# Optimization experiments

Measured on AMD Instinct MI355X. Metric: run time of the kernel, lower is better.

Reference implementation:

```python
import jax, jax.numpy as jnp
import numpy as np

D_X, N_LAYERS, N_HEADS, D_OUT = 1024, 4, 16, 1024
D_H = D_X // N_HEADS
LN_EPS = 1e-5


def _layernorm(x, g, b):
    mu = jnp.mean(x, axis=-1, keepdims=True)
    var = jnp.var(x, axis=-1, keepdims=True)
    return (x - mu) * jax.lax.rsqrt(var + LN_EPS) * g + b


def setup_inputs() -> dict:
    key = jax.random.key(0)
    ks = jax.random.split(key, 12)
    s = 0.02
    inp = {
        "x": jax.random.normal(ks[0], (4, 1024, D_X), dtype=jnp.float32),
        # per-layer, per-head K/V projections (Q is unused by the original math)
        "Wk": jax.random.normal(ks[1], (N_LAYERS, N_HEADS, D_X, D_H), dtype=jnp.float32) * s,
        "bk": jnp.zeros((N_LAYERS, N_HEADS, D_H), dtype=jnp.float32),
        "Wv": jax.random.normal(ks[2], (N_LAYERS, N_HEADS, D_X, D_H), dtype=jnp.float32) * s,
        "bv": jnp.zeros((N_LAYERS, N_HEADS, D_H), dtype=jnp.float32),
        # per-layer FFN linear
        "Wl": jax.random.normal(ks[3], (N_LAYERS, D_X, D_X), dtype=jnp.float32) * s,
        "bl": jnp.zeros((N_LAYERS, D_X), dtype=jnp.float32),
        # per-layer LayerNorm params
        "g1": jnp.ones((N_LAYERS, D_X), dtype=jnp.float32),
        "b1": jnp.zeros((N_LAYERS, D_X), dtype=jnp.float32),
        "g2": jnp.ones((N_LAYERS, D_X), dtype=jnp.float32),
        "b2": jnp.zeros((N_LAYERS, D_X), dtype=jnp.float32),
        # output projection
        "Wo": jax.random.normal(ks[4], (D_X, D_OUT), dtype=jnp.float32) * s,
        "bo": jnp.zeros((D_OUT,), dtype=jnp.float32),
    }
    return inp


def reference(x, Wk, bk, Wv, bv, Wl, bl, g1, b1, g2, b2, Wo, bo):
    B, S, _ = x.shape
    scale = 1.0 / np.sqrt(D_H).astype(np.float32)
    for l in range(N_LAYERS):
        # batched across heads instead of the original per-head Python loop
        K = jnp.einsum("bsd,hdk->bhsk", x, Wk[l]) + bk[l][None, :, None, :]
        V = jnp.einsum("bsd,hdk->bhsk", x, Wv[l]) + bv[l][None, :, None, :]
        # faithful quirk: logits = K @ V^T (Q is never used in the source)
        logits = jnp.einsum("bhsk,bhtk->bhst", K, V) * scale
        attn = jnp.einsum("bhst,bhtk->bhsk", jax.nn.softmax(logits, axis=-1), V)
        attn = attn.transpose(0, 2, 1, 3).reshape(B, S, D_X)  # concat heads
        x = _layernorm(x + attn, g1[l], b1[l])
        ff = jax.nn.relu(jnp.einsum("bsd,de->bse", x, Wl[l]) + bl[l])
        x = _layernorm(x + ff, g2[l], b2[l])
    return jnp.einsum("bsd,do->bso", x, Wo) + bo
```

## Files before the change

### kernel.cpp

```cpp
#include <hip/hip_runtime.h>

typedef unsigned short u16;
typedef unsigned int u32;
typedef __attribute__((ext_vector_type(4))) float f32x4;
typedef __attribute__((ext_vector_type(8))) short short8;

#if __has_builtin(__builtin_amdgcn_exp2f)
#define EXP2(x) __builtin_amdgcn_exp2f(x)
#else
#define EXP2(x) exp2f(x)
#endif

#define SCALEK 0.18033688011112042f

__device__ __forceinline__ u16 f2b(float f) {
    unsigned u = __float_as_uint(f);
    u += 0x7fff + ((u >> 16) & 1);
    return (u16)(u >> 16);
}
__device__ __forceinline__ float b2f(u16 v) {
    return __uint_as_float(((unsigned)v) << 16);
}
__device__ __forceinline__ int swz(int byteoff) {
    return byteoff ^ (((byteoff >> 7) & 7) << 4);
}
__device__ __forceinline__ int swzV(int byteoff) {
    return byteoff ^ (((byteoff >> 8) & 7) << 4);
}
__device__ __forceinline__ void gl16(const u16* g, u16* l) {
    __builtin_amdgcn_global_load_lds(
        (const __attribute__((address_space(1))) unsigned*)(g),
        (__attribute__((address_space(3))) unsigned*)(l), 16, 0, 0);
}
__device__ __forceinline__ u32 cvtpk(float lo, float hi) {
    u32 r;
    asm("v_cvt_pk_bf16_f32 %0, %1, %2" : "=v"(r) : "v"(lo), "v"(hi));
    return r;
}
__device__ __forceinline__ void plswap(u32& a, u32& b) {
    asm("v_permlane32_swap_b32 %0, %1" : "+v"(a), "+v"(b));
    asm("v_permlane16_swap_b32 %0, %1" : "+v"(a), "+v"(b));
}
#define MFMA16(a, b, c) __builtin_amdgcn_mfma_f32_16x16x32_bf16((a), (b), (c), 0, 0, 0)

__global__ __launch_bounds__(256) void pack_wkv_t(const float* __restrict__ W,
                                                  u16* __restrict__ out, int voff) {
    __shared__ float tile[32][33];
    int z = blockIdx.z; int l = z >> 4, h = z & 15;
    const float* ip = W + (size_t)z * 1024 * 64;
    u16* op = out + (size_t)l * 2048 * 1024 + (size_t)(voff + h * 64) * 1024;
    int tx = threadIdx.x & 31, ty = threadIdx.x >> 5;
    int d0 = blockIdx.y * 32, k0 = blockIdx.x * 32;
#pragma unroll
    for (int j = 0; j < 32; j += 8)
        tile[ty + j][tx] = ip[(size_t)(d0 + ty + j) * 64 + k0 + tx];
    __syncthreads();
#pragma unroll
    for (int j = 0; j < 32; j += 8)
        op[(size_t)(k0 + ty + j) * 1024 + d0 + tx] = f2b(tile[tx][ty + j]);
}

__global__ __launch_bounds__(256) void transpose_cvt(const float* __restrict__ in,
                                                     u16* __restrict__ out, int R, int C) {
    __shared__ float tile[32][33];
    const float* ip = in + (size_t)blockIdx.z * R * C;
    u16* op = out + (size_t)blockIdx.z * R * C;
    int tx = threadIdx.x & 31, ty = threadIdx.x >> 5;
    int r0 = blockIdx.y * 32, c0 = blockIdx.x * 32;
#pragma unroll
    for (int j = 0; j < 32; j += 8)
        tile[ty + j][tx] = ip[(size_t)(r0 + ty + j) * C + c0 + tx];
    __syncthreads();
#pragma unroll
    for (int j = 0; j < 32; j += 8)
        op[(size_t)(c0 + ty + j) * R + r0 + tx] = f2b(tile[tx][ty + j]);
}

__global__ __launch_bounds__(256) void cvt_bf16(const float* __restrict__ in,
                                                u16* __restrict__ out, int n) {
    int i = (blockIdx.x * 256 + threadIdx.x) * 4;
    if (i >= n) return;
    float4 v = *(const float4*)&in[i];
    ushort4 o = {f2b(v.x), f2b(v.y), f2b(v.z), f2b(v.w)};
    *(ushort4*)&out[i] = o;
}

template <int EPI, int BN>
__global__ __launch_bounds__(256) void gemm_bt(const u16* __restrict__ A,
                                               const u16* __restrict__ B,
                                               const float* __restrict__ bias1,
                                               const float* __restrict__ bias2, int split,
                                               void* __restrict__ Cv,
                                               u16* __restrict__ VTout,
                                               int M, int N, int K) {
    constexpr int NB = BN / 32;
    constexpr int NLB = BN / 32;
    constexpr int L2BN = (BN == 128) ? 7 : 6;
    __shared__ __align__(16) u16 lA[2][128 * 64];
    __shared__ __align__(16) u16 lB[2][BN * 64];
    const int t = threadIdx.x;
    const int lane = t & 63, w = t >> 6;
    const int wr = w >> 1, wc = w & 1;
    const int g = lane >> 4, r = lane & 15;
    const int bid = blockIdx.x;
    const int rgn = bid & 7, idx = bid >> 3;
    const int by = (rgn >> 1) * 8 + (idx >> 3);
    const int bx = (rgn & 1) * 8 + (idx & 7);
    const int m0 = by * 128, n0 = bx * BN;

    const u16* sA[4];
    const u16* sB[NLB];
#pragma unroll
    for (int j = 0; j < 4; ++j) {
        int c = j * 256 + t;
        sA[j] = A + (size_t)(m0 + (c & 127)) * K + (c >> 7) * 8;
    }
#pragma unroll
    for (int j = 0; j < NLB; ++j) {
        int c = j * 256 + t;
        sB[j] = B + (size_t)(n0 + (c & (BN - 1))) * K + (c >> L2BN) * 8;
    }

    f32x4 zero4 = {0.f, 0.f, 0.f, 0.f};
    f32x4 acc[4][NB];
#pragma unroll
    for (int m = 0; m < 4; ++m)
#pragma unroll
        for (int n = 0; n < NB; ++n) acc[m][n] = zero4;

#define GSTAGE(bufi, k0)                                                 \
    do {                                                                 \
        _Pragma("unroll") for (int j = 0; j < 4; ++j)                    \
            gl16(sA[j] + (k0), &lA[bufi][(j * 256 + w * 64) * 8]);       \
        _Pragma("unroll") for (int j = 0; j < NLB; ++j)                  \
            gl16(sB[j] + (k0), &lB[bufi][(j * 256 + w * 64) * 8]);       \
    } while (0)

    GSTAGE(0, 0);
    __syncthreads();
    const int nk = K >> 6;
    for (int kt = 0; kt < nk; ++kt) {
        const int cur = kt & 1;
        if (kt + 1 < nk) GSTAGE(cur ^ 1, (kt + 1) * 64);
#pragma unroll
        for (int ks = 0; ks < 2; ++ks) {
            short8 af[4], bf[NB];
#pragma unroll
            for (int m = 0; m < 4; ++m)
                af[m] = *(const short8*)&lA[cur][((ks * 4 + g) * 128 + wr * 64 + m * 16 + r) * 8];
#pragma unroll
            for (int n = 0; n < NB; ++n)
                bf[n] = *(const short8*)&lB[cur][((ks * 4 + g) * BN + wc * (BN / 2) + n * 16 + r) * 8];
#pragma unroll
            for (int m = 0; m < 4; ++m)
#pragma unroll
                for (int n = 0; n < NB; ++n)
                    acc[m][n] = MFMA16(af[m], bf[n], acc[m][n]);
        }
        __syncthreads();
    }
#undef GSTAGE

#pragma unroll
    for (int m = 0; m < 4; ++m) {
        int row = m0 + wr * 64 + m * 16 + g * 4;
#pragma unroll
        for (int n = 0; n < NB; ++n) {
            int col = n0 + wc * (BN / 2) + n * 16 + r;
            float bv_ = (col < split) ? bias1[col] : bias2[col - split];
            if (EPI == 0) {
                float sc = (col < split) ? SCALEK : 1.0f;
                ushort4 qv;
                qv.x = f2b((acc[m][n][0] + bv_) * sc);
                qv.y = f2b((acc[m][n][1] + bv_) * sc);
                qv.z = f2b((acc[m][n][2] + bv_) * sc);
                qv.w = f2b((acc[m][n][3] + bv_) * sc);
                u16* Cb = (u16*)Cv;
                Cb[(size_t)(row + 0) * N + col] = qv.x;
                Cb[(size_t)(row + 1) * N + col] = qv.y;
                Cb[(size_t)(row + 2) * N + col] = qv.z;
                Cb[(size_t)(row + 3) * N + col] = qv.w;
                if (col >= split) {
                    int d = col - split, b_ = row >> 10, s = row & 1023;
                    *(ushort4*)&VTout[(((size_t)(b_ * 16) + (d >> 6)) * 64 + (d & 63)) * 1024 + s] = qv;
                }
            } else if (EPI == 1) {
                u16* Cb = (u16*)Cv;
#pragma unroll
                for (int i = 0; i < 4; ++i)
                    Cb[(size_t)(row + i) * N + col] = f2b(fmaxf(acc[m][n][i] + bv_, 0.f));
            } else {
#pragma unroll
                for (int i = 0; i < 4; ++i)
                    ((float*)Cv)[(size_t)(row + i) * N + col] = acc[m][n][i] + bv_;
            }
        }
    }
}

__global__ __launch_bounds__(512) void attn_kernel(const u16* __restrict__ KV,
                                                   const u16* __restrict__ VT,
                                                   u16* __restrict__ Out) {
    __shared__ __align__(16) u16 kt[2][1024 * 8];
    __shared__ __align__(16) u16 vt[2][1024 * 8];
    const int t = threadIdx.x;
    const int lane = t & 63, w = t >> 6;
    const int g = lane >> 4, r = lane & 15;
    const int d0 = blockIdx.x;
    const int q = d0 >> 3;
    const int bh = (d0 & 7) * 8 + (q >> 3), qb = q & 7;
    const int h = bh & 15, b = bh >> 4;
    const u16* Kbase = KV + (size_t)b * 1024 * 2048 + h * 64;
    const u16* Vbase = Kbase + 1024;
    const u16* VTbase = VT + ((size_t)(b * 16 + h)) * 64 * 1024;

    const int qrow = qb * 128 + w * 16 + r;
    const short8 qf0 = *(const short8*)&Kbase[(size_t)qrow * 2048 + g * 8];
    const short8 qf1 = *(const short8*)&Kbase[(size_t)qrow * 2048 + 32 + g * 8];

    const int krow1 = t >> 3;
    const int kcol = ((((t & 7) * 16) ^ ((krow1 & 7) << 4)) >> 1);
    const u16* Ks1 = Vbase + (size_t)krow1 * 2048 + kcol;
    const u16* Ks2 = Vbase + (size_t)(64 + krow1) * 2048 + kcol;
    const int vrow1 = t >> 4;
    const int vcol = ((((t & 15) * 16) ^ ((vrow1 & 7) << 4)) >> 1);
    const u16* Vs1 = VTbase + (size_t)vrow1 * 1024 + vcol;
    const u16* Vs2 = VTbase + (size_t)(32 + vrow1) * 1024 + vcol;

#define STAGE(bufi, t0)                                              \
    do {                                                             \
        gl16(Ks1 + (size_t)(t0) * 2048, &kt[bufi][(w * 64) * 8]);    \
        gl16(Ks2 + (size_t)(t0) * 2048, &kt[bufi][(512 + w * 64) * 8]); \
        gl16(Vs1 + (t0), &vt[bufi][(w * 64) * 8]);                   \
        gl16(Vs2 + (t0), &vt[bufi][(512 + w * 64) * 8]);             \
    } while (0)

    STAGE(0, 0);

    float m = -1e30f, l = 0.f;
    f32x4 zero4 = {0.f, 0.f, 0.f, 0.f};
    f32x4 oacc[4];
#pragma unroll
    for (int n = 0; n < 4; ++n) oacc[n] = zero4;
    const int cbase = (lane & 48) | (g << 2);
    __syncthreads();

    for (int tt = 0; tt < 8; ++tt) {
        const int cur = tt & 1;
        if (tt < 7) STAGE(cur ^ 1, (tt + 1) * 128);
        const char* kbuf = (const char*)&kt[cur][0];
        const char* vbuf = (const char*)&vt[cur][0];

        f32x4 sfT[8];
#pragma unroll
        for (int n = 0; n < 8; ++n) sfT[n] = zero4;
#pragma unroll
        for (int ks = 0; ks < 2; ++ks) {
            const short8 qf = ks ? qf1 : qf0;
#pragma unroll
            for (int n = 0; n < 8; ++n) {
                short8 kf = *(const short8*)(kbuf + swz((n * 16 + r) * 128 + ks * 64 + g * 16));
                sfT[n] = MFMA16(kf, qf, sfT[n]);
            }
        }
        float rm = -1e30f;
#pragma unroll
        for (int n = 0; n < 8; ++n)
            rm = fmaxf(rm, fmaxf(fmaxf(sfT[n][0], sfT[n][1]), fmaxf(sfT[n][2], sfT[n][3])));
        rm = fmaxf(rm, __shfl_xor(rm, 16, 64));
        rm = fmaxf(rm, __shfl_xor(rm, 32, 64));
        if (!__all(rm <= m + 8.f)) {
            float mn = fmaxf(m, rm);
            float cc = EXP2(m - mn);
            m = mn;
            l *= cc;
#pragma unroll
            for (int i = 0; i < 4; ++i) {
                float ci = __shfl(cc, cbase + i, 64);
#pragma unroll
                for (int n = 0; n < 4; ++n) oacc[n][i] *= ci;
            }
        }
        float rs = 0.f;
#pragma unroll
        for (int n = 0; n < 8; ++n)
#pragma unroll
            for (int i = 0; i < 4; ++i) {
                float p = EXP2(sfT[n][i] - m);
                sfT[n][i] = p;
                rs += p;
            }
        rs += __shfl_xor(rs, 16, 64);
        rs += __shfl_xor(rs, 32, 64);
        l += rs;
        u32 wpk[8][2];
#pragma unroll
        for (int n = 0; n < 8; ++n) {
            wpk[n][0] = cvtpk(sfT[n][0], sfT[n][1]);
            wpk[n][1] = cvtpk(sfT[n][2], sfT[n][3]);
        }
#pragma unroll
        for (int ks = 0; ks < 4; ++ks) {
            u32 a0 = wpk[2 * ks][0], a2 = wpk[2 * ks + 1][0];
            plswap(a0, a2);
            u32 a1 = wpk[2 * ks][1], a3 = wpk[2 * ks + 1][1];
            plswap(a1, a3);
            uint4 av;
            av.x = a0; av.y = a1; av.z = a2; av.w = a3;
            union { uint4 u; short8 s; } uc;
            uc.u = av;
            const short8 af = uc.s;
#pragma unroll
            for (int n = 0; n < 4; ++n) {
                short8 vf = *(const short8*)(vbuf + swzV((n * 16 + r) * 256 + ks * 64 + g * 16));
                oacc[n] = MFMA16(af, vf, oacc[n]);
            }
        }
        __syncthreads();
    }
#undef STAGE

#pragma unroll
    for (int i = 0; i < 4; ++i) {
        float li = 1.f / __shfl(l, cbase + i, 64);
        int orow = b * 1024 + qb * 128 + w * 16 + g * 4 + i;
#pragma unroll
        for (int n = 0; n < 4; ++n)
            Out[(size_t)orow * 1024 + h * 64 + n * 16 + r] = f2b(oacc[n][i] * li);
    }
}

__global__ __launch_bounds__(256) void ln_kernel(const u16* __restrict__ xin,
                                                 const u16* __restrict__ addin,
                                                 const float* __restrict__ gamma,
                                                 const float* __restrict__ beta,
                                                 u16* __restrict__ xbout) {
    const int row = blockIdx.x, t = threadIdx.x;
    const size_t base = (size_t)row * 1024;
    ushort4 xu = *(const ushort4*)&xin[base + t * 4];
    ushort4 au = *(const ushort4*)&addin[base + t * 4];
    float v0 = b2f(xu.x) + b2f(au.x), v1 = b2f(xu.y) + b2f(au.y);
    float v2 = b2f(xu.z) + b2f(au.z), v3 = b2f(xu.w) + b2f(au.w);
    float s = v0 + v1 + v2 + v3;
    __shared__ float red[4];
    const int lane = t & 63, w = t >> 6;
#pragma unroll
    for (int off = 32; off; off >>= 1) s += __shfl_xor(s, off, 64);
    if (lane == 0) red[w] = s;
    __syncthreads();
    float mean = (red[0] + red[1] + red[2] + red[3]) * (1.f / 1024.f);
    __syncthreads();
    float d0 = v0 - mean, d1 = v1 - mean, d2 = v2 - mean, d3 = v3 - mean;
    float sq = d0 * d0 + d1 * d1 + d2 * d2 + d3 * d3;
#pragma unroll
    for (int off = 32; off; off >>= 1) sq += __shfl_xor(sq, off, 64);
    if (lane == 0) red[w] = sq;
    __syncthreads();
    float var = (red[0] + red[1] + red[2] + red[3]) * (1.f / 1024.f);
    float rstd = rsqrtf(var + 1e-5f);
    float4 gv = *(const float4*)&gamma[t * 4];
    float4 bv = *(const float4*)&beta[t * 4];
    ushort4 o;
    o.x = f2b(d0 * rstd * gv.x + bv.x);
    o.y = f2b(d1 * rstd * gv.y + bv.y);
    o.z = f2b(d2 * rstd * gv.z + bv.z);
    o.w = f2b(d3 * rstd * gv.w + bv.w);
    *(ushort4*)&xbout[base + t * 4] = o;
}

extern "C" void kernel_launch(void* const* d_in, const int* in_sizes, int n_in,
                              void* d_out, int out_size, void* d_ws, size_t ws_size,
                              hipStream_t stream) {
    const float* x  = (const float*)d_in[0];
    const float* Wk = (const float*)d_in[1];
    const float* bk = (const float*)d_in[2];
    const float* Wv = (const float*)d_in[3];
    const float* bv = (const float*)d_in[4];
    const float* Wl = (const float*)d_in[5];
    const float* bl = (const float*)d_in[6];
    const float* g1 = (const float*)d_in[7];
    const float* b1 = (const float*)d_in[8];
    const float* g2 = (const float*)d_in[9];
    const float* b2 = (const float*)d_in[10];
    const float* Wo = (const float*)d_in[11];
    const float* bo = (const float*)d_in[12];

    char* ws = (char*)d_ws;
    u16* Wkvb = (u16*)ws;  ws += (size_t)4 * 2048 * 1024 * 2;
    u16* Wlb  = (u16*)ws;  ws += (size_t)4 * 1024 * 1024 * 2;
    u16* Wob  = (u16*)ws;  ws += (size_t)1024 * 1024 * 2;
    u16* xb   = (u16*)ws;  ws += (size_t)4096 * 1024 * 2;
    u16* KVb  = (u16*)ws;  ws += (size_t)4096 * 2048 * 2;
    u16* VTb  = (u16*)ws;  ws += (size_t)4096 * 1024 * 2;
    u16* tmpb = (u16*)ws;  ws += (size_t)4096 * 1024 * 2;

    pack_wkv_t<<<dim3(2, 32, 64), 256, 0, stream>>>(Wk, Wkvb, 0);
    pack_wkv_t<<<dim3(2, 32, 64), 256, 0, stream>>>(Wv, Wkvb, 1024);
    transpose_cvt<<<dim3(32, 32, 4), 256, 0, stream>>>(Wl, Wlb, 1024, 1024);
    transpose_cvt<<<dim3(32, 32, 1), 256, 0, stream>>>(Wo, Wob, 1024, 1024);
    cvt_bf16<<<dim3(4096), 256, 0, stream>>>(x, xb, 4096 * 1024);

    for (int l = 0; l < 4; ++l) {
        gemm_bt<0, 128><<<dim3(512), 256, 0, stream>>>(
            xb, Wkvb + (size_t)l * 2048 * 1024, bk + l * 1024, bv + l * 1024, 1024,
            (void*)KVb, VTb, 4096, 2048, 1024);
        attn_kernel<<<dim3(512), 512, 0, stream>>>(KVb, VTb, tmpb);
        ln_kernel<<<dim3(4096), 256, 0, stream>>>(
            xb, tmpb, g1 + l * 1024, b1 + l * 1024, xb);
        gemm_bt<1, 64><<<dim3(512), 256, 0, stream>>>(
            xb, Wlb + (size_t)l * 1024 * 1024, bl + l * 1024, bl + l * 1024, 1024,
            (void*)tmpb, nullptr, 4096, 1024, 1024);
        ln_kernel<<<dim3(4096), 256, 0, stream>>>(
            xb, tmpb, g2 + l * 1024, b2 + l * 1024, xb);
    }
    gemm_bt<2, 64><<<dim3(512), 256, 0, stream>>>(
        xb, Wob, bo, bo, 1024, d_out, nullptr, 4096, 1024, 1024);
}
```

Baseline: 494.0 us.

## Use 8 waves per GEMM block with K-step 32 and halved LDS tiles

Reworks the GEMM kernel to launch 512 threads (8 waves in a 2x4 grid) per block instead of 256, so each wave computes a narrower column slice. The K tile shrinks from 64 to 32, which halves shared memory per stage and lets each thread issue a single global-to-LDS load per stage. The aim is more waves per CU for latency hiding and lower LDS footprint. In exchange there are twice as many loop iterations and barriers, and each wave does fewer MFMAs per fragment load, which lowers operand reuse.

```diff
diff --git a/kernel.cpp b/kernel.cpp
--- a/kernel.cpp
+++ b/kernel.cpp
@@ -86,21 +86,19 @@
 }
 
 template <int EPI, int BN>
-__global__ __launch_bounds__(256) void gemm_bt(const u16* __restrict__ A,
+__global__ __launch_bounds__(512) void gemm_bt(const u16* __restrict__ A,
                                                const u16* __restrict__ B,
                                                const float* __restrict__ bias1,
                                                const float* __restrict__ bias2, int split,
                                                void* __restrict__ Cv,
                                                u16* __restrict__ VTout,
                                                int M, int N, int K) {
-    constexpr int NB = BN / 32;
-    constexpr int NLB = BN / 32;
-    constexpr int L2BN = (BN == 128) ? 7 : 6;
-    __shared__ __align__(16) u16 lA[2][128 * 64];
-    __shared__ __align__(16) u16 lB[2][BN * 64];
+    constexpr int NBW = BN / 64;
+    __shared__ __align__(16) u16 lA[2][512 * 8];
+    __shared__ __align__(16) u16 lB[2][BN * 4 * 8];
     const int t = threadIdx.x;
     const int lane = t & 63, w = t >> 6;
-    const int wr = w >> 1, wc = w & 1;
+    const int wr = w >> 2, wc = w & 3;
     const int g = lane >> 4, r = lane & 15;
     const int bid = blockIdx.x;
     const int rgn = bid & 7, idx = bid >> 3;
@@ -108,55 +106,42 @@
     const int bx = (rgn & 1) * 8 + (idx & 7);
     const int m0 = by * 128, n0 = bx * BN;
 
-    const u16* sA[4];
-    const u16* sB[NLB];
-#pragma unroll
-    for (int j = 0; j < 4; ++j) {
-        int c = j * 256 + t;
-        sA[j] = A + (size_t)(m0 + (c & 127)) * K + (c >> 7) * 8;
-    }
-#pragma unroll
-    for (int j = 0; j < NLB; ++j) {
-        int c = j * 256 + t;
-        sB[j] = B + (size_t)(n0 + (c & (BN - 1))) * K + (c >> L2BN) * 8;
-    }
+    const u16* sA = A + (size_t)(m0 + (t & 127)) * K + (t >> 7) * 8;
+    const int cB = (BN == 128) ? t : (t & 255);
+    const u16* sB = B + (size_t)(n0 + (cB & (BN - 1))) * K + (cB / BN) * 8;
 
     f32x4 zero4 = {0.f, 0.f, 0.f, 0.f};
-    f32x4 acc[4][NB];
+    f32x4 acc[4][NBW];
 #pragma unroll
     for (int m = 0; m < 4; ++m)
 #pragma unroll
-        for (int n = 0; n < NB; ++n) acc[m][n] = zero4;
-
-#define GSTAGE(bufi, k0)                                                 \
-    do {                                                                 \
-        _Pragma("unroll") for (int j = 0; j < 4; ++j)                    \
-            gl16(sA[j] + (k0), &lA[bufi][(j * 256 + w * 64) * 8]);       \
-        _Pragma("unroll") for (int j = 0; j < NLB; ++j)                  \
-            gl16(sB[j] + (k0), &lB[bufi][(j * 256 + w * 64) * 8]);       \
+        for (int n = 0; n < NBW; ++n) acc[m][n] = zero4;
+
+#define GSTAGE(bufi, k0)                                           \
+    do {                                                           \
+        gl16(sA + (k0), &lA[bufi][(w * 64) * 8]);                  \
+        if (BN == 128 || w < 4)                                    \
+            gl16(sB + (k0), &lB[bufi][(w * 64) * 8]);              \
     } while (0)
 
     GSTAGE(0, 0);
     __syncthreads();
-    const int nk = K >> 6;
+    const int nk = K >> 5;
     for (int kt = 0; kt < nk; ++kt) {
         const int cur = kt & 1;
-        if (kt + 1 < nk) GSTAGE(cur ^ 1, (kt + 1) * 64);
-#pragma unroll
-        for (int ks = 0; ks < 2; ++ks) {
-            short8 af[4], bf[NB];
-#pragma unroll
-            for (int m = 0; m < 4; ++m)
-                af[m] = *(const short8*)&lA[cur][((ks * 4 + g) * 128 + wr * 64 + m * 16 + r) * 8];
-#pragma unroll
-            for (int n = 0; n < NB; ++n)
-                bf[n] = *(const short8*)&lB[cur][((ks * 4 + g) * BN + wc * (BN / 2) + n * 16 + r) * 8];
-#pragma unroll
-            for (int m = 0; m < 4; ++m)
-#pragma unroll
-                for (int n = 0; n < NB; ++n)
-                    acc[m][n] = MFMA16(af[m], bf[n], acc[m][n]);
-        }
+        if (kt + 1 < nk) GSTAGE(cur ^ 1, (kt + 1) * 32);
+        short8 af[4], bf[NBW];
+#pragma unroll
+        for (int m = 0; m < 4; ++m)
+            af[m] = *(const short8*)&lA[cur][(g * 128 + wr * 64 + m * 16 + r) * 8];
+#pragma unroll
+        for (int n = 0; n < NBW; ++n)
+            bf[n] = *(const short8*)&lB[cur][(g * BN + wc * (BN / 4) + n * 16 + r) * 8];
+#pragma unroll
+        for (int m = 0; m < 4; ++m)
+#pragma unroll
+            for (int n = 0; n < NBW; ++n)
+                acc[m][n] = MFMA16(af[m], bf[n], acc[m][n]);
         __syncthreads();
     }
 #undef GSTAGE
@@ -165,8 +150,8 @@
     for (int m = 0; m < 4; ++m) {
         int row = m0 + wr * 64 + m * 16 + g * 4;
 #pragma unroll
-        for (int n = 0; n < NB; ++n) {
-            int col = n0 + wc * (BN / 2) + n * 16 + r;
+        for (int n = 0; n < NBW; ++n) {
+            int col = n0 + wc * (BN / 4) + n * 16 + r;
             float bv_ = (col < split) ? bias1[col] : bias2[col - split];
             if (EPI == 0) {
                 float sc = (col < split) ? SCALEK : 1.0f;
@@ -401,18 +386,18 @@
     cvt_bf16<<<dim3(4096), 256, 0, stream>>>(x, xb, 4096 * 1024);
 
     for (int l = 0; l < 4; ++l) {
-        gemm_bt<0, 128><<<dim3(512), 256, 0, stream>>>(
+        gemm_bt<0, 128><<<dim3(512), 512, 0, stream>>>(
             xb, Wkvb + (size_t)l * 2048 * 1024, bk + l * 1024, bv + l * 1024, 1024,
             (void*)KVb, VTb, 4096, 2048, 1024);
         attn_kernel<<<dim3(512), 512, 0, stream>>>(KVb, VTb, tmpb);
         ln_kernel<<<dim3(4096), 256, 0, stream>>>(
             xb, tmpb, g1 + l * 1024, b1 + l * 1024, xb);
-        gemm_bt<1, 64><<<dim3(512), 256, 0, stream>>>(
+        gemm_bt<1, 64><<<dim3(512), 512, 0, stream>>>(
             xb, Wlb + (size_t)l * 1024 * 1024, bl + l * 1024, bl + l * 1024, 1024,
             (void*)tmpb, nullptr, 4096, 1024, 1024);
         ln_kernel<<<dim3(4096), 256, 0, stream>>>(
             xb, tmpb, g2 + l * 1024, b2 + l * 1024, xb);
     }
-    gemm_bt<2, 64><<<dim3(512), 256, 0, stream>>>(
+    gemm_bt<2, 64><<<dim3(512), 512, 0, stream>>>(
         xb, Wob, bo, bo, 1024, d_out, nullptr, 4096, 1024, 1024);
 }
```

New measurement: 504.5 us. +2.1%, slower.

## Quantize K/V projection GEMM to int8 with per-row scales

Applied to the files above, without the earlier changes.

Replaces the bf16 K/V projection GEMM with an int8 MFMA GEMM that uses per-row symmetric scales for both activations and packed weights. Weights are quantized once after packing. Activations are quantized in the input conversion and in the second LayerNorm of each layer, so the next layer's GEMM reads int8. The aim is to double MFMA throughput and halve operand bytes for the largest per-layer GEMM, at the cost of int8 rounding error on K and V. It also adds an extra reduction and write in the LayerNorm.

```diff
diff --git a/kernel.cpp b/kernel.cpp
--- a/kernel.cpp
+++ b/kernel.cpp
@@ -2,7 +2,9 @@
 
 typedef unsigned short u16;
 typedef unsigned int u32;
+typedef signed char i8;
 typedef __attribute__((ext_vector_type(4))) float f32x4;
+typedef __attribute__((ext_vector_type(4))) int i32x4;
 typedef __attribute__((ext_vector_type(8))) short short8;
 
 #if __has_builtin(__builtin_amdgcn_exp2f)
@@ -27,7 +29,7 @@
 __device__ __forceinline__ int swzV(int byteoff) {
     return byteoff ^ (((byteoff >> 8) & 7) << 4);
 }
-__device__ __forceinline__ void gl16(const u16* g, u16* l) {
+__device__ __forceinline__ void gl16(const void* g, void* l) {
     __builtin_amdgcn_global_load_lds(
         (const __attribute__((address_space(1))) unsigned*)(g),
         (__attribute__((address_space(3))) unsigned*)(l), 16, 0, 0);
@@ -41,7 +43,22 @@
     asm("v_permlane32_swap_b32 %0, %1" : "+v"(a), "+v"(b));
     asm("v_permlane16_swap_b32 %0, %1" : "+v"(a), "+v"(b));
 }
+__device__ __forceinline__ void up8(uint4 u, float* v) {
+    v[0] = b2f((u16)u.x); v[1] = b2f((u16)(u.x >> 16));
+    v[2] = b2f((u16)u.y); v[3] = b2f((u16)(u.y >> 16));
+    v[4] = b2f((u16)u.z); v[5] = b2f((u16)(u.z >> 16));
+    v[6] = b2f((u16)u.w); v[7] = b2f((u16)(u.w >> 16));
+}
+__device__ __forceinline__ int qclamp(float v) {
+    int q = __float2int_rn(v);
+    return (q > 127) ? 127 : ((q < -127) ? -127 : q);
+}
+__device__ __forceinline__ u32 pk4(int a, int b, int c, int d) {
+    return (u32)(unsigned char)a | ((u32)(unsigned char)b << 8) |
+           ((u32)(unsigned char)c << 16) | ((u32)(unsigned char)d << 24);
+}
 #define MFMA16(a, b, c) __builtin_amdgcn_mfma_f32_16x16x32_bf16((a), (b), (c), 0, 0, 0)
+#define MFMAI8(a, b, c) __builtin_amdgcn_mfma_i32_16x16x64_i8((a), (b), (c), 0, 0, 0)
 
 __global__ __launch_bounds__(256) void pack_wkv_t(const float* __restrict__ W,
                                                   u16* __restrict__ out, int voff) {
@@ -76,13 +93,161 @@
         op[(size_t)(c0 + ty + j) * R + r0 + tx] = f2b(tile[tx][ty + j]);
 }
 
-__global__ __launch_bounds__(256) void cvt_bf16(const float* __restrict__ in,
-                                                u16* __restrict__ out, int n) {
-    int i = (blockIdx.x * 256 + threadIdx.x) * 4;
-    if (i >= n) return;
-    float4 v = *(const float4*)&in[i];
-    ushort4 o = {f2b(v.x), f2b(v.y), f2b(v.z), f2b(v.w)};
-    *(ushort4*)&out[i] = o;
+__global__ __launch_bounds__(256) void quant_rows(const u16* __restrict__ in,
+                                                  i8* __restrict__ out,
+                                                  float* __restrict__ scale) {
+    const int t = threadIdx.x, lane = t & 63, w = t >> 6;
+    const int row = blockIdx.x * 4 + w;
+    const size_t base = (size_t)row * 1024 + lane * 16;
+    uint4 v0 = *(const uint4*)&in[base];
+    uint4 v1 = *(const uint4*)&in[base + 8];
+    float v[16];
+    up8(v0, v); up8(v1, v + 8);
+    float amax = 0.f;
+#pragma unroll
+    for (int i = 0; i < 16; ++i) amax = fmaxf(amax, fabsf(v[i]));
+#pragma unroll
+    for (int off = 32; off; off >>= 1) amax = fmaxf(amax, __shfl_xor(amax, off, 64));
+    const float inv = (amax > 0.f) ? 127.f / amax : 0.f;
+    u32 q[4];
+#pragma unroll
+    for (int j = 0; j < 4; ++j)
+        q[j] = pk4(qclamp(v[4 * j] * inv), qclamp(v[4 * j + 1] * inv),
+                   qclamp(v[4 * j + 2] * inv), qclamp(v[4 * j + 3] * inv));
+    uint4 qq = {q[0], q[1], q[2], q[3]};
+    *(uint4*)&out[base] = qq;
+    if (lane == 0) scale[row] = (amax > 0.f) ? amax / 127.f : 0.f;
+}
+
+__global__ __launch_bounds__(256) void cvtq_row(const float* __restrict__ in,
+                                                u16* __restrict__ outb,
+                                                i8* __restrict__ outq,
+                                                float* __restrict__ scale) {
+    const int t = threadIdx.x, lane = t & 63, w = t >> 6;
+    const int row = blockIdx.x * 4 + w;
+    const size_t base = (size_t)row * 1024 + lane * 16;
+    float v[16];
+#pragma unroll
+    for (int j = 0; j < 4; ++j) {
+        float4 f = *(const float4*)&in[base + j * 4];
+        v[4 * j] = f.x; v[4 * j + 1] = f.y; v[4 * j + 2] = f.z; v[4 * j + 3] = f.w;
+    }
+    u32 bw[8];
+#pragma unroll
+    for (int j = 0; j < 8; ++j) bw[j] = cvtpk(v[2 * j], v[2 * j + 1]);
+    uint4 b0 = {bw[0], bw[1], bw[2], bw[3]};
+    uint4 b1 = {bw[4], bw[5], bw[6], bw[7]};
+    *(uint4*)&outb[base] = b0;
+    *(uint4*)&outb[base + 8] = b1;
+    float amax = 0.f;
+#pragma unroll
+    for (int i = 0; i < 16; ++i) amax = fmaxf(amax, fabsf(v[i]));
+#pragma unroll
+    for (int off = 32; off; off >>= 1) amax = fmaxf(amax, __shfl_xor(amax, off, 64));
+    const float inv = (amax > 0.f) ? 127.f / amax : 0.f;
+    u32 q[4];
+#pragma unroll
+    for (int j = 0; j < 4; ++j)
+        q[j] = pk4(qclamp(v[4 * j] * inv), qclamp(v[4 * j + 1] * inv),
+                   qclamp(v[4 * j + 2] * inv), qclamp(v[4 * j + 3] * inv));
+    uint4 qq = {q[0], q[1], q[2], q[3]};
+    *(uint4*)&outq[base] = qq;
+    if (lane == 0) scale[row] = (amax > 0.f) ? amax / 127.f : 0.f;
+}
+
+__global__ __launch_bounds__(256) void gemm_kv_i8(const i8* __restrict__ A,
+                                                  const float* __restrict__ sA,
+                                                  const i8* __restrict__ B,
+                                                  const float* __restrict__ sB,
+                                                  const float* __restrict__ bias1,
+                                                  const float* __restrict__ bias2,
+                                                  u16* __restrict__ Cb,
+                                                  u16* __restrict__ VTout) {
+    constexpr int K = 1024, N = 2048;
+    __shared__ __align__(16) i8 lA[2][8 * 128 * 16];
+    __shared__ __align__(16) i8 lB[2][8 * 128 * 16];
+    const int t = threadIdx.x;
+    const int lane = t & 63, w = t >> 6;
+    const int wr = w >> 1, wc = w & 1;
+    const int g = lane >> 4, r = lane & 15;
+    const int bid = blockIdx.x;
+    const int rgn = bid & 7, idx = bid >> 3;
+    const int by = (rgn >> 1) * 8 + (idx >> 3);
+    const int bx = (rgn & 1) * 8 + (idx & 7);
+    const int m0 = by * 128, n0 = bx * 128;
+
+    const i8* sAp[4];
+    const i8* sBp[4];
+#pragma unroll
+    for (int j = 0; j < 4; ++j) {
+        int c = j * 256 + t;
+        sAp[j] = A + (size_t)(m0 + (c & 127)) * K + (c >> 7) * 16;
+        sBp[j] = B + (size_t)(n0 + (c & 127)) * K + (c >> 7) * 16;
+    }
+
+    i32x4 acc[4][4];
+#pragma unroll
+    for (int m = 0; m < 4; ++m)
+#pragma unroll
+        for (int n = 0; n < 4; ++n) acc[m][n] = (i32x4){0, 0, 0, 0};
+
+#define GSTAGE(bufi, k0)                                                  \
+    do {                                                                  \
+        _Pragma("unroll") for (int j = 0; j < 4; ++j)                     \
+            gl16(sAp[j] + (k0), &lA[bufi][(j * 256 + w * 64) * 16]);      \
+        _Pragma("unroll") for (int j = 0; j < 4; ++j)                     \
+            gl16(sBp[j] + (k0), &lB[bufi][(j * 256 + w * 64) * 16]);      \
+    } while (0)
+
+    GSTAGE(0, 0);
+    __syncthreads();
+    for (int kt = 0; kt < 8; ++kt) {
+        const int cur = kt & 1;
+        if (kt + 1 < 8) GSTAGE(cur ^ 1, (kt + 1) * 128);
+#pragma unroll
+        for (int ks = 0; ks < 2; ++ks) {
+            i32x4 af[4], bf[4];
+#pragma unroll
+            for (int m = 0; m < 4; ++m)
+                af[m] = *(const i32x4*)&lA[cur][((ks * 4 + g) * 128 + wr * 64 + m * 16 + r) * 16];
+#pragma unroll
+            for (int n = 0; n < 4; ++n)
+                bf[n] = *(const i32x4*)&lB[cur][((ks * 4 + g) * 128 + wc * 64 + n * 16 + r) * 16];
+#pragma unroll
+            for (int m = 0; m < 4; ++m)
+#pragma unroll
+                for (int n = 0; n < 4; ++n)
+                    acc[m][n] = MFMAI8(af[m], bf[n], acc[m][n]);
+        }
+        __syncthreads();
+    }
+#undef GSTAGE
+
+#pragma unroll
+    for (int m = 0; m < 4; ++m) {
+        int row = m0 + wr * 64 + m * 16 + g * 4;
+        float sx0 = sA[row], sx1 = sA[row + 1], sx2 = sA[row + 2], sx3 = sA[row + 3];
+#pragma unroll
+        for (int n = 0; n < 4; ++n) {
+            int col = n0 + wc * 64 + n * 16 + r;
+            float swv = sB[col];
+            float bv_ = (col < 1024) ? bias1[col] : bias2[col - 1024];
+            float sc = (col < 1024) ? SCALEK : 1.0f;
+            ushort4 qv;
+            qv.x = f2b(((float)acc[m][n][0] * sx0 * swv + bv_) * sc);
+            qv.y = f2b(((float)acc[m][n][1] * sx1 * swv + bv_) * sc);
+            qv.z = f2b(((float)acc[m][n][2] * sx2 * swv + bv_) * sc);
+            qv.w = f2b(((float)acc[m][n][3] * sx3 * swv + bv_) * sc);
+            Cb[(size_t)(row + 0) * N + col] = qv.x;
+            Cb[(size_t)(row + 1) * N + col] = qv.y;
+            Cb[(size_t)(row + 2) * N + col] = qv.z;
+            Cb[(size_t)(row + 3) * N + col] = qv.w;
+            if (col >= 1024) {
+                int d = col - 1024, b_ = row >> 10, s = row & 1023;
+                *(ushort4*)&VTout[(((size_t)(b_ * 16) + (d >> 6)) * 64 + (d & 63)) * 1024 + s] = qv;
+            }
+        }
+    }
 }
 
 template <int EPI, int BN>
@@ -91,7 +256,6 @@
                                                const float* __restrict__ bias1,
                                                const float* __restrict__ bias2, int split,
                                                void* __restrict__ Cv,
-                                               u16* __restrict__ VTout,
                                                int M, int N, int K) {
     constexpr int NB = BN / 32;
     constexpr int NLB = BN / 32;
@@ -168,23 +332,7 @@
         for (int n = 0; n < NB; ++n) {
             int col = n0 + wc * (BN / 2) + n * 16 + r;
             float bv_ = (col < split) ? bias1[col] : bias2[col - split];
-            if (EPI == 0) {
-                float sc = (col < split) ? SCALEK : 1.0f;
-                ushort4 qv;
-                qv.x = f2b((acc[m][n][0] + bv_) * sc);
-                qv.y = f2b((acc[m][n][1] + bv_) * sc);
-                qv.z = f2b((acc[m][n][2] + bv_) * sc);
-                qv.w = f2b((acc[m][n][3] + bv_) * sc);
-                u16* Cb = (u16*)Cv;
-                Cb[(size_t)(row + 0) * N + col] = qv.x;
-                Cb[(size_t)(row + 1) * N + col] = qv.y;
-                Cb[(size_t)(row + 2) * N + col] = qv.z;
-                Cb[(size_t)(row + 3) * N + col] = qv.w;
-                if (col >= split) {
-                    int d = col - split, b_ = row >> 10, s = row & 1023;
-                    *(ushort4*)&VTout[(((size_t)(b_ * 16) + (d >> 6)) * 64 + (d & 63)) * 1024 + s] = qv;
-                }
-            } else if (EPI == 1) {
+            if (EPI == 1) {
                 u16* Cb = (u16*)Cv;
 #pragma unroll
                 for (int i = 0; i < 4; ++i)
@@ -330,11 +478,14 @@
     }
 }
 
+template <int QOUT>
 __global__ __launch_bounds__(256) void ln_kernel(const u16* __restrict__ xin,
                                                  const u16* __restrict__ addin,
                                                  const float* __restrict__ gamma,
                                                  const float* __restrict__ beta,
-                                                 u16* __restrict__ xbout) {
+                                                 u16* __restrict__ xbout,
+                                                 i8* __restrict__ xq,
+                                                 float* __restrict__ sx) {
     const int row = blockIdx.x, t = threadIdx.x;
     const size_t base = (size_t)row * 1024;
     ushort4 xu = *(const ushort4*)&xin[base + t * 4];
@@ -360,12 +511,26 @@
     float rstd = rsqrtf(var + 1e-5f);
     float4 gv = *(const float4*)&gamma[t * 4];
     float4 bv = *(const float4*)&beta[t * 4];
+    float o0 = d0 * rstd * gv.x + bv.x;
+    float o1 = d1 * rstd * gv.y + bv.y;
+    float o2 = d2 * rstd * gv.z + bv.z;
+    float o3 = d3 * rstd * gv.w + bv.w;
     ushort4 o;
-    o.x = f2b(d0 * rstd * gv.x + bv.x);
-    o.y = f2b(d1 * rstd * gv.y + bv.y);
-    o.z = f2b(d2 * rstd * gv.z + bv.z);
-    o.w = f2b(d3 * rstd * gv.w + bv.w);
+    o.x = f2b(o0); o.y = f2b(o1); o.z = f2b(o2); o.w = f2b(o3);
     *(ushort4*)&xbout[base + t * 4] = o;
+    if (QOUT) {
+        float am = fmaxf(fmaxf(fabsf(o0), fabsf(o1)), fmaxf(fabsf(o2), fabsf(o3)));
+#pragma unroll
+        for (int off = 32; off; off >>= 1) am = fmaxf(am, __shfl_xor(am, off, 64));
+        __syncthreads();
+        if (lane == 0) red[w] = am;
+        __syncthreads();
+        float amax = fmaxf(fmaxf(red[0], red[1]), fmaxf(red[2], red[3]));
+        float inv = (amax > 0.f) ? 127.f / amax : 0.f;
+        u32 qw = pk4(qclamp(o0 * inv), qclamp(o1 * inv), qclamp(o2 * inv), qclamp(o3 * inv));
+        *(u32*)&xq[base + t * 4] = qw;
+        if (t == 0) sx[row] = (amax > 0.f) ? amax / 127.f : 0.f;
+    }
 }
 
 extern "C" void kernel_launch(void* const* d_in, const int* in_sizes, int n_in,
@@ -393,26 +558,31 @@
     u16* KVb  = (u16*)ws;  ws += (size_t)4096 * 2048 * 2;
     u16* VTb  = (u16*)ws;  ws += (size_t)4096 * 1024 * 2;
     u16* tmpb = (u16*)ws;  ws += (size_t)4096 * 1024 * 2;
+    i8*  Wq   = (i8*)ws;   ws += (size_t)4 * 2048 * 1024;
+    i8*  xq   = (i8*)ws;   ws += (size_t)4096 * 1024;
+    float* swf = (float*)ws; ws += (size_t)4 * 2048 * 4;
+    float* sxf = (float*)ws; ws += (size_t)4096 * 4;
 
     pack_wkv_t<<<dim3(2, 32, 64), 256, 0, stream>>>(Wk, Wkvb, 0);
     pack_wkv_t<<<dim3(2, 32, 64), 256, 0, stream>>>(Wv, Wkvb, 1024);
+    quant_rows<<<dim3(2048), 256, 0, stream>>>(Wkvb, Wq, swf);
     transpose_cvt<<<dim3(32, 32, 4), 256, 0, stream>>>(Wl, Wlb, 1024, 1024);
     transpose_cvt<<<dim3(32, 32, 1), 256, 0, stream>>>(Wo, Wob, 1024, 1024);
-    cvt_bf16<<<dim3(4096), 256, 0, stream>>>(x, xb, 4096 * 1024);
+    cvtq_row<<<dim3(1024), 256, 0, stream>>>(x, xb, xq, sxf);
 
     for (int l = 0; l < 4; ++l) {
-        gemm_bt<0, 128><<<dim3(512), 256, 0, stream>>>(
-            xb, Wkvb + (size_t)l * 2048 * 1024, bk + l * 1024, bv + l * 1024, 1024,
-            (void*)KVb, VTb, 4096, 2048, 1024);
+        gemm_kv_i8<<<dim3(512), 256, 0, stream>>>(
+            xq, sxf, Wq + (size_t)l * 2048 * 1024, swf + l * 2048,
+            bk + l * 1024, bv + l * 1024, KVb, VTb);
         attn_kernel<<<dim3(512), 512, 0, stream>>>(KVb, VTb, tmpb);
-        ln_kernel<<<dim3(4096), 256, 0, stream>>>(
-            xb, tmpb, g1 + l * 1024, b1 + l * 1024, xb);
+        ln_kernel<0><<<dim3(4096), 256, 0, stream>>>(
+            xb, tmpb, g1 + l * 1024, b1 + l * 1024, xb, nullptr, nullptr);
         gemm_bt<1, 64><<<dim3(512), 256, 0, stream>>>(
             xb, Wlb + (size_t)l * 1024 * 1024, bl + l * 1024, bl + l * 1024, 1024,
-            (void*)tmpb, nullptr, 4096, 1024, 1024);
-        ln_kernel<<<dim3(4096), 256, 0, stream>>>(
-            xb, tmpb, g2 + l * 1024, b2 + l * 1024, xb);
+            (void*)tmpb, 4096, 1024, 1024);
+        ln_kernel<1><<<dim3(4096), 256, 0, stream>>>(
+            xb, tmpb, g2 + l * 1024, b2 + l * 1024, xb, xq, sxf);
     }
     gemm_bt<2, 64><<<dim3(512), 256, 0, stream>>>(
-        xb, Wob, bo, bo, 1024, d_out, nullptr, 4096, 1024, 1024);
-}
+        xb, Wob, bo, bo, 1024, d_out, 4096, 1024, 1024);
+}
```

New measurement: 456.2 us. 7.6% less time.
